# Kernel tuning notes

Measured on AMD Instinct MI355X. Metric: run time of the kernel, lower is better.

Reference implementation:

```python
import jax, jax.numpy as jnp
import numpy as np

B, N, M, D = 2, 16384, 4096, 128  # batch, points, voxels, d_model (= d_points)


def _mlp(x, W1, b1, W2, b2):
    # Linear -> ReLU -> Linear (matches nn.Sequential(Linear, ReLU, Linear))
    return jax.nn.relu(x @ W1 + b1) @ W2 + b2


def setup_inputs() -> dict:
    key = jax.random.key(0)
    ks = jax.random.split(key, 12)
    s = 0.02
    inp = {
        "p_xyz": jax.random.normal(ks[0], (B, N, 3), jnp.float32),
        "v_xyz": jax.random.normal(ks[1], (B, 3), jnp.float32),
        "p_features": jax.random.normal(ks[2], (B, N, D), jnp.float32),
        "v_featrues": jax.random.normal(ks[3], (B, M, D), jnp.float32),
    }

    def two_layer(k, din):
        k1, k2 = jax.random.split(k)
        return (jax.random.normal(k1, (din, D), jnp.float32) * s,
                jnp.zeros((D,), jnp.float32),
                jax.random.normal(k2, (D, D), jnp.float32) * s,
                jnp.zeros((D,), jnp.float32))

    for name, din, k in (("alpha", D, ks[4]), ("beta", D, ks[5]),
                         ("omega", D, ks[6]), ("delta", 3, ks[7])):
        W1, b1, W2, b2 = two_layer(k, din)
        inp[name + "_W1"] = W1
        inp[name + "_b1"] = b1
        inp[name + "_W2"] = W2
        inp[name + "_b2"] = b2
    return inp


def reference(p_xyz, v_xyz, p_features, v_featrues,
              alpha_W1, alpha_b1, alpha_W2, alpha_b2,
              beta_W1, beta_b1, beta_W2, beta_b2,
              omega_W1, omega_b1, omega_W2, omega_b2,
              delta_W1, delta_b1, delta_W2, delta_b2):
    # dist = |p_xyz - v_xyz| per batch: [B, N, 3]
    dist = jnp.abs(p_xyz - v_xyz[:, None, :])
    pv = _mlp(dist, delta_W1, delta_b1, delta_W2, delta_b2)        # [B, N, D]
    q = _mlp(v_featrues, alpha_W1, alpha_b1, alpha_W2, alpha_b2)   # [B, M, D]
    k = _mlp(p_features, beta_W1, beta_b1, beta_W2, beta_b2)       # [B, N, D]
    v = _mlp(p_features, omega_W1, omega_b1, omega_W2, omega_b2)   # [B, N, D]
    # q@k^T + q@pv^T == q@(k+pv)^T : [B, M, N]
    scale = 1.0 / jnp.sqrt(jnp.asarray(D, dtype=q.dtype))
    scores = jnp.einsum('bmd,bnd->bmn', q, k + pv) * scale
    # softmax over dim=-2 (the query/voxel dim M), as in the original
    w = jax.nn.softmax(scores, axis=-2)                            # [B, M, N]
    res = jnp.einsum('bmn,bnd->bmd', w, v)                         # [B, M, D]
    return res + v_featrues
```

## Files before the change

### kernel.cpp

```cpp
#include <hip/hip_runtime.h>

#define B_ 2
#define N_ 16384
#define M_ 4096
#define D_ 128

typedef __attribute__((ext_vector_type(8))) short s8;
typedef __attribute__((ext_vector_type(4))) float f4;
typedef __attribute__((ext_vector_type(16))) float f16v;
typedef __attribute__((ext_vector_type(4))) unsigned short us4;
typedef unsigned short u16;

__device__ __forceinline__ u16 f2b(float f) {
  unsigned int x = __float_as_uint(f);
  unsigned int r = x + 0x7fffu + ((x >> 16) & 1u);
  return (u16)(r >> 16);
}
__device__ __forceinline__ s8 ld8(const u16* p) {
  return *reinterpret_cast<const s8*>(p);
}
__device__ __forceinline__ s8 ldcvt8(const float* p) {
  f4 x = *reinterpret_cast<const f4*>(p);
  f4 y = *reinterpret_cast<const f4*>(p + 4);
  s8 r;
  r[0] = (short)f2b(x[0]); r[1] = (short)f2b(x[1]);
  r[2] = (short)f2b(x[2]); r[3] = (short)f2b(x[3]);
  r[4] = (short)f2b(y[0]); r[5] = (short)f2b(y[1]);
  r[6] = (short)f2b(y[2]); r[7] = (short)f2b(y[3]);
  return r;
}
__device__ __forceinline__ f4 mfma16(s8 a, s8 b, f4 c) {
  return __builtin_amdgcn_mfma_f32_16x16x32_bf16(a, b, c, 0, 0, 0);
}
__device__ __forceinline__ f16v mfma32(s8 a, s8 b, f16v c) {
  return __builtin_amdgcn_mfma_f32_32x32x16_bf16(a, b, c, 0, 0, 0);
}
__device__ __forceinline__ int swz(int row, int off) {
  return (row << 8) + ((((off >> 4) ^ (row & 15)) << 4) | (off & 15));
}
#define CS 0.1275174365f

__device__ __forceinline__ void lds_barrier() {
  asm volatile("s_waitcnt lgkmcnt(0)" ::: "memory");
  __builtin_amdgcn_s_barrier();
}

__global__ __launch_bounds__(256) void wtrans(
    const float* a0, const float* a1, const float* a2, const float* a3,
    const float* a4, const float* a5, const float* a6, u16* dst) {
  const int mat = blockIdx.x >> 4, part = blockIdx.x & 15;
  const float* s;
  switch (mat) {
    case 0: s = a0; break; case 1: s = a1; break; case 2: s = a2; break;
    case 3: s = a3; break; case 4: s = a4; break; case 5: s = a5; break;
    default: s = a6; break;
  }
  u16* d = dst + mat * 16384 + part * 1024;
  const int o0 = part * 1024;
  for (int i = threadIdx.x; i < 1024; i += 256) {
    const int o = o0 + i;
    const int c = o >> 7, r = o & 127;
    d[i] = f2b(s[r * 128 + c]);
  }
}

__global__ __launch_bounds__(256) void mlps(
    const float* __restrict__ vfeat,
    const u16* __restrict__ aW1t, const float* __restrict__ ab1,
    const u16* __restrict__ aW2t, const float* __restrict__ ab2,
    u16* __restrict__ qbuf,
    const float* __restrict__ pf, const float* __restrict__ pxyz,
    const float* __restrict__ vxyz,
    const u16* __restrict__ bW1t, const float* __restrict__ bb1,
    const u16* __restrict__ bW2t, const float* __restrict__ bb2,
    const float* __restrict__ dW1, const float* __restrict__ db1,
    const u16* __restrict__ dW2t, const float* __restrict__ db2,
    const u16* __restrict__ oW1t, const float* __restrict__ ob1,
    const u16* __restrict__ oW2t, const float* __restrict__ ob2,
    u16* __restrict__ kpv_out, u16* __restrict__ vt_out) {
  __shared__ u16 H1[64][136];
  __shared__ u16 H2[64][136];
  __shared__ u16 H3[64][136];
  const int tid = threadIdx.x;
  const int wave = tid >> 6, lane = tid & 63;
  const int c16 = lane & 15, quad = lane >> 4;

  if (blockIdx.x < 256) {
    const int rowg = wave & 1, nsh = wave >> 1;
    const long row0 = (long)blockIdx.x * 32 + rowg * 16;
    s8 a[4];
    {
      const float* xr = vfeat + (row0 + c16) * D_ + quad * 8;
      #pragma unroll
      for (int kk = 0; kk < 4; kk++) a[kk] = ldcvt8(xr + kk * 32);
    }
    #pragma unroll
    for (int ns = 0; ns < 4; ns++) {
      f4 acc = {0.f, 0.f, 0.f, 0.f};
      const int c = (nsh * 4 + ns) * 16 + c16;
      const u16* wr = aW1t + (long)c * 128 + quad * 8;
      #pragma unroll
      for (int kk = 0; kk < 4; kk++) acc = mfma16(a[kk], ld8(wr + kk * 32), acc);
      const float bias = ab1[c];
      #pragma unroll
      for (int r = 0; r < 4; r++) {
        float v = acc[r] + bias;
        H1[rowg * 16 + quad * 4 + r][c] = f2b(v > 0.f ? v : 0.f);
      }
    }
    __syncthreads();
    s8 a2[4];
    #pragma unroll
    for (int kk = 0; kk < 4; kk++)
      a2[kk] = *reinterpret_cast<const s8*>(&H1[rowg * 16 + c16][kk * 32 + quad * 8]);
    #pragma unroll
    for (int ns = 0; ns < 4; ns++) {
      f4 acc = {0.f, 0.f, 0.f, 0.f};
      const int c = (nsh * 4 + ns) * 16 + c16;
      const u16* wr = aW2t + (long)c * 128 + quad * 8;
      #pragma unroll
      for (int kk = 0; kk < 4; kk++) acc = mfma16(a2[kk], ld8(wr + kk * 32), acc);
      const float bias = ab2[c];
      #pragma unroll
      for (int r = 0; r < 4; r++)
        qbuf[(row0 + quad * 4 + r) * D_ + c] = f2b(acc[r] + bias);
    }
    return;
  }
  const int bx = blockIdx.x - 256;
  const long row0 = (long)bx * 64 + wave * 16;
  s8 a[4];
  {
    const float* xr = pf + (row0 + c16) * D_ + quad * 8;
    #pragma unroll
    for (int kk = 0; kk < 4; kk++) a[kk] = ldcvt8(xr + kk * 32);
  }
  #pragma unroll
  for (int ns = 0; ns < 8; ns++) {
    f4 accb = {0.f, 0.f, 0.f, 0.f}, acco = {0.f, 0.f, 0.f, 0.f};
    const int c = ns * 16 + c16;
    const u16* wrb = bW1t + (long)c * 128 + quad * 8;
    const u16* wro = oW1t + (long)c * 128 + quad * 8;
    #pragma unroll
    for (int kk = 0; kk < 4; kk++) {
      accb = mfma16(a[kk], ld8(wrb + kk * 32), accb);
      acco = mfma16(a[kk], ld8(wro + kk * 32), acco);
    }
    const float biasb = bb1[c], biaso = ob1[c];
    #pragma unroll
    for (int r = 0; r < 4; r++) {
      float vb = accb[r] + biasb;
      float vo = acco[r] + biaso;
      H1[wave * 16 + quad * 4 + r][c] = f2b(vb > 0.f ? vb : 0.f);
      H3[wave * 16 + quad * 4 + r][c] = f2b(vo > 0.f ? vo : 0.f);
    }
  }
  {
    const long bat = ((long)bx * 64) / N_;
    const float vx0 = vxyz[bat * 3 + 0];
    const float vx1 = vxyz[bat * 3 + 1];
    const float vx2 = vxyz[bat * 3 + 2];
    for (int i = 0; i < 32; i++) {
      const int e = lane + 64 * i;
      const int rr = e >> 7, cc = e & 127;
      const long gr = row0 + rr;
      const float d0 = fabsf(pxyz[gr * 3 + 0] - vx0);
      const float d1 = fabsf(pxyz[gr * 3 + 1] - vx1);
      const float d2 = fabsf(pxyz[gr * 3 + 2] - vx2);
      float h = d0 * dW1[cc] + d1 * dW1[128 + cc] + d2 * dW1[256 + cc] + db1[cc];
      H2[wave * 16 + rr][cc] = f2b(h > 0.f ? h : 0.f);
    }
  }
  __syncthreads();
  s8 ab[4], ad[4], ao[4];
  #pragma unroll
  for (int kk = 0; kk < 4; kk++) {
    ab[kk] = *reinterpret_cast<const s8*>(&H1[wave * 16 + c16][kk * 32 + quad * 8]);
    ad[kk] = *reinterpret_cast<const s8*>(&H2[wave * 16 + c16][kk * 32 + quad * 8]);
    ao[kk] = *reinterpret_cast<const s8*>(&H3[wave * 16 + c16][kk * 32 + quad * 8]);
  }
  #pragma unroll
  for (int ns = 0; ns < 8; ns++) {
    const int c = ns * 16 + c16;
    f4 acck = {0.f, 0.f, 0.f, 0.f};
    f4 accv = {0.f, 0.f, 0.f, 0.f};
    const u16* wrb = bW2t + (long)c * 128 + quad * 8;
    const u16* wrd = dW2t + (long)c * 128 + quad * 8;
    const u16* wro = oW2t + (long)c * 128 + quad * 8;
    #pragma unroll
    for (int kk = 0; kk < 4; kk++) {
      acck = mfma16(ab[kk], ld8(wrb + kk * 32), acck);
      acck = mfma16(ad[kk], ld8(wrd + kk * 32), acck);
      accv = mfma16(ao[kk], ld8(wro + kk * 32), accv);
    }
    const float biask = bb2[c] + db2[c];
    const float biasv = ob2[c];
    #pragma unroll
    for (int r = 0; r < 4; r++)
      kpv_out[(row0 + quad * 4 + r) * D_ + c] = f2b(acck[r] + biask);
    {
      const long g = row0 + quad * 4;
      const long bb = g >> 14;
      const long n = g & (N_ - 1);
      us4 pk;
      #pragma unroll
      for (int r = 0; r < 4; r++) pk[r] = f2b(accv[r] + biasv);
      *reinterpret_cast<us4*>(vt_out + bb * (long)128 * N_ + (long)c * N_ + n) = pk;
    }
  }
}

__global__ __launch_bounds__(512, 4) void colsum_v3(const u16* __restrict__ q,
    const u16* __restrict__ kpv, float* __restrict__ sums) {
  __shared__ char LQ[2][32768];
  const int tid = threadIdx.x;
  const int wave = tid >> 6, lane = tid & 63;
  const int c16 = lane & 15, quad = lane >> 4;
  const int mh = blockIdx.x & 3;
  const int nb = ((blockIdx.x >> 2) & 127) * 128 + wave * 16;
  const int b = blockIdx.x >> 9;
  const int rsub = lane >> 4, ch = lane & 15;

  s8 ak[4];
  {
    const u16* kr = kpv + ((long)b * N_ + nb + c16) * D_ + quad * 8;
    #pragma unroll
    for (int kk = 0; kk < 4; kk++) ak[kk] = ld8(kr + kk * 32);
  }
  f4 sum = {0.f, 0.f, 0.f, 0.f};
  const u16* qb = q + (long)b * M_ * D_ + (long)mh * (M_ / 4) * D_;

  s8 t[4];
  #pragma unroll
  for (int i = 0; i < 4; i++)
    t[i] = ld8(qb + (long)(wave * 16 + i * 4 + rsub) * D_ + ch * 8);
  #pragma unroll
  for (int i = 0; i < 4; i++)
    *reinterpret_cast<s8*>(LQ[0] + swz(wave * 16 + i * 4 + rsub, ch * 16)) = t[i];

  for (int s = 0; s < 8; s++) {
    lds_barrier();
    const int m1 = (s + 1) * 128;
    if (s < 7) {
      #pragma unroll
      for (int i = 0; i < 4; i++)
        t[i] = ld8(qb + (long)(m1 + wave * 16 + i * 4 + rsub) * D_ + ch * 8);
    }
    const char* lq = LQ[s & 1];
    #pragma unroll
    for (int ms = 0; ms < 8; ms++) {
      f4 st = {0.f, 0.f, 0.f, 0.f};
      #pragma unroll
      for (int kk = 0; kk < 4; kk++) {
        s8 bq = *reinterpret_cast<const s8*>(lq + swz(ms * 16 + c16, kk * 64 + quad * 16));
        st = mfma16(ak[kk], bq, st);
      }
      #pragma unroll
      for (int r = 0; r < 4; r++) sum[r] += exp2f(st[r] * CS);
    }
    if (s < 7) {
      #pragma unroll
      for (int i = 0; i < 4; i++)
        *reinterpret_cast<s8*>(LQ[(s + 1) & 1]
            + swz(wave * 16 + i * 4 + rsub, ch * 16)) = t[i];
    }
  }
  #pragma unroll
  for (int mask = 1; mask < 16; mask <<= 1) {
    #pragma unroll
    for (int r = 0; r < 4; r++) sum[r] += __shfl_xor(sum[r], mask, 64);
  }
  if (c16 == 0)
    *reinterpret_cast<f4*>(sums + (long)mh * (B_ * N_) + (long)b * N_ + nb + quad * 4) = sum;
}

__global__ __launch_bounds__(256) void recip_k(const float* __restrict__ sums,
                                               float* __restrict__ l2ic) {
  const int i = blockIdx.x * 256 + threadIdx.x;
  const float s = sums[i] + sums[B_ * N_ + i] + sums[2 * B_ * N_ + i]
                + sums[3 * B_ * N_ + i];
  l2ic[i] = -log2f(s);
}

__global__ __launch_bounds__(256, 2) void attn_v13(const u16* __restrict__ q,
    const u16* __restrict__ kpv, const u16* __restrict__ vt,
    const float* __restrict__ l2ic, float* __restrict__ part,
    int lgns, int nslice) {
  __shared__ char LK[16384];
  __shared__ char LP[16384];
  const int tid = threadIdx.x;
  const int wave = tid >> 6, lane = tid & 63;
  const int l31 = lane & 31, hi = lane >> 5;
  const int bid = blockIdx.x;
  const int ns = bid & ((1 << lgns) - 1);
  const int mb = (bid >> lgns) & 31;
  const int b = bid >> (lgns + 5);
  const int nt = wave & 1, mth = wave >> 1;
  const int m_base = mb * 128;
  const int n_begin = ns * nslice;
  const int rsub = lane >> 4, ch = lane & 15;

  const u16* kpb = kpv + (long)b * N_ * D_;
  const u16* vtb = vt + (long)b * (long)D_ * N_;
  const float* l2b = l2ic + (long)b * N_;

  s8 bq[2][8];
  #pragma unroll
  for (int t = 0; t < 2; t++) {
    const u16* qr = q + ((long)b * M_ + m_base + (mth + 2 * t) * 32 + l31) * D_ + hi * 8;
    #pragma unroll
    for (int kk = 0; kk < 8; kk++) bq[t][kk] = ld8(qr + kk * 16);
  }
  f16v acc[4];
  #pragma unroll
  for (int i = 0; i < 4; i++)
    #pragma unroll
    for (int r = 0; r < 16; r++) acc[i][r] = 0.f;

  s8 tmp[4];
  #pragma unroll
  for (int i = 0; i < 4; i++)
    tmp[i] = ld8(kpb + (long)(n_begin + wave * 16 + i * 4 + rsub) * D_ + ch * 8);

  for (int n0 = n_begin; n0 < n_begin + nslice; n0 += 64) {
    #pragma unroll
    for (int i = 0; i < 4; i++)
      *reinterpret_cast<s8*>(LK + swz(wave * 16 + i * 4 + rsub, ch * 16)) = tmp[i];
    {
      int nn = n0 + 64;
      if (nn >= n_begin + nslice) nn = n_begin;
      #pragma unroll
      for (int i = 0; i < 4; i++)
        tmp[i] = ld8(kpb + (long)(nn + wave * 16 + i * 4 + rsub) * D_ + ch * 8);
    }
    lds_barrier();
    s8 bv[4];
    #pragma unroll
    for (int kk = 0; kk < 4; kk++)
      bv[kk] = ld8(vtb + (long)(wave * 32 + l31) * N_ + n0 + kk * 16 + hi * 8);
    {
      f16v st0, st1;
      #pragma unroll
      for (int r = 0; r < 16; r++) { st0[r] = 0.f; st1[r] = 0.f; }
      #pragma unroll
      for (int kk = 0; kk < 8; kk++) {
        s8 aK = *reinterpret_cast<const s8*>(
            LK + swz(nt * 32 + l31, kk * 32 + hi * 16));
        st0 = mfma32(aK, bq[0][kk], st0);
        st1 = mfma32(aK, bq[1][kk], st1);
      }
      #pragma unroll
      for (int g = 0; g < 4; g++) {
        const f4 l2 = *reinterpret_cast<const f4*>(l2b + n0 + nt * 32 + 8 * g + 4 * hi);
        us4 pk0, pk1;
        #pragma unroll
        for (int r = 0; r < 4; r++) {
          pk0[r] = (u16)(__float_as_uint(exp2f(fmaf(st0[g * 4 + r], CS, l2[r]))) >> 16);
          pk1[r] = (u16)(__float_as_uint(exp2f(fmaf(st1[g * 4 + r], CS, l2[r]))) >> 16);
        }
        *reinterpret_cast<us4*>(LP + (4 * nt + g) * 2048
                                + ((mth + 0) * 32 + l31) * 16 + 8 * hi) = pk0;
        *reinterpret_cast<us4*>(LP + (4 * nt + g) * 2048
                                + ((mth + 2) * 32 + l31) * 16 + 8 * hi) = pk1;
      }
    }
    lds_barrier();
    #pragma unroll
    for (int kk = 0; kk < 4; kk++) {
      #pragma unroll
      for (int i = 0; i < 4; i++) {
        s8 ap = *reinterpret_cast<const s8*>(
            LP + (2 * kk + hi) * 2048 + (i * 32 + l31) * 16);
        acc[i] = mfma32(ap, bv[kk], acc[i]);
      }
    }
  }
  float* pt = part + (long)bid * 128 * 128;
  #pragma unroll
  for (int i = 0; i < 4; i++)
    #pragma unroll
    for (int g = 0; g < 4; g++)
      #pragma unroll
      for (int r = 0; r < 4; r++)
        pt[(i * 32 + g * 8 + 4 * hi + r) * 128 + wave * 32 + l31] = acc[i][g * 4 + r];
}

__global__ __launch_bounds__(256) void attn_reduce(const float* __restrict__ part,
    const float* __restrict__ vfeat, float* __restrict__ out, int nsplit) {
  const int g4 = blockIdx.x * 256 + threadIdx.x;
  const int b = g4 >> 17;
  const int rem = g4 & 131071;
  const int m = rem >> 5;
  const int d4 = rem & 31;
  const int mb = m >> 7, mr = m & 127;
  const long base = ((long)(b * 32 + mb) * nsplit) * 16384 + mr * 128 + d4 * 4;
  f4 s = *reinterpret_cast<const f4*>(vfeat + (long)g4 * 4);
  for (int ns = 0; ns < nsplit; ns++)
    s += *reinterpret_cast<const f4*>(part + base + ns * 16384);
  *reinterpret_cast<f4*>(out + (long)g4 * 4) = s;
}

extern "C" void kernel_launch(void* const* d_in, const int* in_sizes, int n_in,
                              void* d_out, int out_size, void* d_ws, size_t ws_size,
                              hipStream_t stream) {
  const float* p_xyz  = (const float*)d_in[0];
  const float* v_xyz  = (const float*)d_in[1];
  const float* p_feat = (const float*)d_in[2];
  const float* v_feat = (const float*)d_in[3];
  const float* aW1 = (const float*)d_in[4],  *ab1 = (const float*)d_in[5];
  const float* aW2 = (const float*)d_in[6],  *ab2 = (const float*)d_in[7];
  const float* bW1 = (const float*)d_in[8],  *bb1 = (const float*)d_in[9];
  const float* bW2 = (const float*)d_in[10], *bb2 = (const float*)d_in[11];
  const float* oW1 = (const float*)d_in[12], *ob1 = (const float*)d_in[13];
  const float* oW2 = (const float*)d_in[14], *ob2 = (const float*)d_in[15];
  const float* dW1 = (const float*)d_in[16], *db1 = (const float*)d_in[17];
  const float* dW2 = (const float*)d_in[18], *db2 = (const float*)d_in[19];

  char* ws = (char*)d_ws;
  u16* wt    = (u16*)ws;
  u16* aW1t  = wt + 0 * 16384;
  u16* aW2t  = wt + 1 * 16384;
  u16* bW1t  = wt + 2 * 16384;
  u16* bW2t  = wt + 3 * 16384;
  u16* oW1t  = wt + 4 * 16384;
  u16* oW2t  = wt + 5 * 16384;
  u16* dW2t  = wt + 6 * 16384;
  u16* qbuf  = (u16*)(ws + 262144);
  u16* kpvb  = (u16*)(ws + 2359296);
  u16* vtb   = (u16*)(ws + 10747904);
  float* invb = (float*)(ws + 19136512);
  float* partb = (float*)(ws + 19267584);
  float* sums  = partb;

  const size_t part_off = 19267584;
  int lgns = (ws_size >= part_off + (size_t)8 * B_ * M_ * D_ * 4) ? 3 : 2;
  const int nsplit = 1 << lgns;
  const int nslice = N_ / nsplit;

  wtrans<<<dim3(112), dim3(256), 0, stream>>>(aW1, aW2, bW1, bW2, oW1, oW2, dW2, wt);
  mlps<<<dim3(256 + (B_ * N_) / 64), dim3(256), 0, stream>>>(
      v_feat, aW1t, ab1, aW2t, ab2, qbuf,
      p_feat, p_xyz, v_xyz, bW1t, bb1, bW2t, bb2, dW1, db1, dW2t, db2,
      oW1t, ob1, oW2t, ob2, kpvb, vtb);
  colsum_v3<<<dim3(B_ * 128 * 4), dim3(512), 0, stream>>>(qbuf, kpvb, sums);
  recip_k<<<dim3((B_ * N_) / 256), dim3(256), 0, stream>>>(sums, invb);
  attn_v13<<<dim3(B_ * 32 * nsplit), dim3(256), 0, stream>>>(qbuf, kpvb, vtb, invb,
                                                             partb, lgns, nslice);
  attn_reduce<<<dim3((B_ * M_ * D_ / 4) / 256), dim3(256), 0, stream>>>(partb, v_feat,
                                                                        (float*)d_out,
                                                                        nsplit);
}
```

Baseline: 292.4 us.

## Double-buffer K and P tiles in LDS to drop one barrier per iteration

The attention kernel now keeps two LDS buffers each for the K tile and the probability tile. The P·V MFMAs of the previous iteration are interleaved with the score computation of the current one, leaving a single barrier per iteration instead of two. This is meant to let the exp/softmax work overlap with MFMA work and cut synchronisation stalls. LDS use doubles to 64 KB per block, which may limit occupancy under the 2-blocks-per-CU launch bound, and register pressure rises because the previous V fragment is carried between iterations.

```diff
diff --git a/kernel.cpp b/kernel.cpp
--- a/kernel.cpp
+++ b/kernel.cpp
@@ -282,12 +282,12 @@
   l2ic[i] = -log2f(s);
 }
 
-__global__ __launch_bounds__(256, 2) void attn_v13(const u16* __restrict__ q,
+__global__ __launch_bounds__(256, 2) void attn_v14(const u16* __restrict__ q,
     const u16* __restrict__ kpv, const u16* __restrict__ vt,
     const float* __restrict__ l2ic, float* __restrict__ part,
     int lgns, int nslice) {
-  __shared__ char LK[16384];
-  __shared__ char LP[16384];
+  __shared__ char LK0[16384], LK1[16384];
+  __shared__ char LP0[16384], LP1[16384];
   const int tid = threadIdx.x;
   const int wave = tid >> 6, lane = tid & 63;
   const int l31 = lane & 31, hi = lane >> 5;
@@ -321,23 +321,26 @@
   #pragma unroll
   for (int i = 0; i < 4; i++)
     tmp[i] = ld8(kpb + (long)(n_begin + wave * 16 + i * 4 + rsub) * D_ + ch * 8);
-
-  for (int n0 = n_begin; n0 < n_begin + nslice; n0 += 64) {
-    #pragma unroll
-    for (int i = 0; i < 4; i++)
-      *reinterpret_cast<s8*>(LK + swz(wave * 16 + i * 4 + rsub, ch * 16)) = tmp[i];
-    {
-      int nn = n0 + 64;
-      if (nn >= n_begin + nslice) nn = n_begin;
-      #pragma unroll
-      for (int i = 0; i < 4; i++)
-        tmp[i] = ld8(kpb + (long)(nn + wave * 16 + i * 4 + rsub) * D_ + ch * 8);
-    }
+  #pragma unroll
+  for (int i = 0; i < 4; i++)
+    *reinterpret_cast<s8*>(LK0 + swz(wave * 16 + i * 4 + rsub, ch * 16)) = tmp[i];
+  #pragma unroll
+  for (int i = 0; i < 4; i++)
+    tmp[i] = ld8(kpb + (long)(n_begin + 64 + wave * 16 + i * 4 + rsub) * D_ + ch * 8);
+
+  const int niter = nslice >> 6;
+  s8 bvp[4];
+  for (int it = 0; it < niter; ++it) {
+    const int n0 = n_begin + it * 64;
+    char* lkc = (it & 1) ? LK1 : LK0;
+    char* lkn = (it & 1) ? LK0 : LK1;
+    char* lpc = (it & 1) ? LP1 : LP0;
+    char* lpp = (it & 1) ? LP0 : LP1;
     lds_barrier();
-    s8 bv[4];
+    s8 bvc[4];
     #pragma unroll
     for (int kk = 0; kk < 4; kk++)
-      bv[kk] = ld8(vtb + (long)(wave * 32 + l31) * N_ + n0 + kk * 16 + hi * 8);
+      bvc[kk] = ld8(vtb + (long)(wave * 32 + l31) * N_ + n0 + kk * 16 + hi * 8);
     {
       f16v st0, st1;
       #pragma unroll
@@ -345,7 +348,7 @@
       #pragma unroll
       for (int kk = 0; kk < 8; kk++) {
         s8 aK = *reinterpret_cast<const s8*>(
-            LK + swz(nt * 32 + l31, kk * 32 + hi * 16));
+            lkc + swz(nt * 32 + l31, kk * 32 + hi * 16));
         st0 = mfma32(aK, bq[0][kk], st0);
         st1 = mfma32(aK, bq[1][kk], st1);
       }
@@ -358,20 +361,46 @@
           pk0[r] = (u16)(__float_as_uint(exp2f(fmaf(st0[g * 4 + r], CS, l2[r]))) >> 16);
           pk1[r] = (u16)(__float_as_uint(exp2f(fmaf(st1[g * 4 + r], CS, l2[r]))) >> 16);
         }
-        *reinterpret_cast<us4*>(LP + (4 * nt + g) * 2048
+        *reinterpret_cast<us4*>(lpc + (4 * nt + g) * 2048
                                 + ((mth + 0) * 32 + l31) * 16 + 8 * hi) = pk0;
-        *reinterpret_cast<us4*>(LP + (4 * nt + g) * 2048
+        *reinterpret_cast<us4*>(lpc + (4 * nt + g) * 2048
                                 + ((mth + 2) * 32 + l31) * 16 + 8 * hi) = pk1;
       }
     }
-    lds_barrier();
+    if (it) {
+      #pragma unroll
+      for (int kk = 0; kk < 4; kk++) {
+        #pragma unroll
+        for (int i = 0; i < 4; i++) {
+          s8 ap = *reinterpret_cast<const s8*>(
+              lpp + (2 * kk + hi) * 2048 + (i * 32 + l31) * 16);
+          acc[i] = mfma32(ap, bvp[kk], acc[i]);
+        }
+      }
+    }
+    #pragma unroll
+    for (int i = 0; i < 4; i++)
+      *reinterpret_cast<s8*>(lkn + swz(wave * 16 + i * 4 + rsub, ch * 16)) = tmp[i];
+    {
+      int nn = n0 + 128;
+      if (nn >= n_begin + nslice) nn = n_begin;
+      #pragma unroll
+      for (int i = 0; i < 4; i++)
+        tmp[i] = ld8(kpb + (long)(nn + wave * 16 + i * 4 + rsub) * D_ + ch * 8);
+    }
+    #pragma unroll
+    for (int kk = 0; kk < 4; kk++) bvp[kk] = bvc[kk];
+  }
+  lds_barrier();
+  {
+    char* lpl = ((niter - 1) & 1) ? LP1 : LP0;
     #pragma unroll
     for (int kk = 0; kk < 4; kk++) {
       #pragma unroll
       for (int i = 0; i < 4; i++) {
         s8 ap = *reinterpret_cast<const s8*>(
-            LP + (2 * kk + hi) * 2048 + (i * 32 + l31) * 16);
-        acc[i] = mfma32(ap, bv[kk], acc[i]);
+            lpl + (2 * kk + hi) * 2048 + (i * 32 + l31) * 16);
+        acc[i] = mfma32(ap, bvp[kk], acc[i]);
       }
     }
   }
@@ -444,7 +473,7 @@
       oW1t, ob1, oW2t, ob2, kpvb, vtb);
   colsum_v3<<<dim3(B_ * 128 * 4), dim3(512), 0, stream>>>(qbuf, kpvb, sums);
   recip_k<<<dim3((B_ * N_) / 256), dim3(256), 0, stream>>>(sums, invb);
-  attn_v13<<<dim3(B_ * 32 * nsplit), dim3(256), 0, stream>>>(qbuf, kpvb, vtb, invb,
+  attn_v14<<<dim3(B_ * 32 * nsplit), dim3(256), 0, stream>>>(qbuf, kpvb, vtb, invb,
                                                              partb, lgns, nslice);
   attn_reduce<<<dim3((B_ * M_ * D_ / 4) / 256), dim3(256), 0, stream>>>(partb, v_feat,
                                                                         (float*)d_out,
```

Result: slower. 307.6 us (+5.2%).
